# Optimization experiments

Hardware: AMD Instinct MI355X
Metric: run time of the kernel (lower is better)

The kernel has to match this reference:

```python
import jax, jax.numpy as jnp
import numpy as np

DIM = 192
NUM_HEADS = 4
B, H, W = 2, 256, 256
EPS = 1e-12  # torch F.normalize default eps


def setup_inputs() -> dict:
    key = jax.random.key(0)
    k1, k2, k3 = jax.random.split(key, 3)
    x = jax.random.normal(k1, (B, DIM, H, W), dtype=jnp.float32)
    # depthwise qkv conv: groups=DIM, each group maps 1 in-ch -> 3 out-ch; torch OIHW layout (3*DIM, 1, 3, 3)
    w_qkv = jax.random.normal(k2, (3 * DIM, 1, 3, 3), dtype=jnp.float32) * 0.1
    temperature = jnp.ones((NUM_HEADS, 1, 1), dtype=jnp.float32)
    # 1x1 projection conv, stored as [out, in]
    w_proj = jax.random.normal(k3, (DIM, DIM), dtype=jnp.float32) * (1.0 / np.sqrt(DIM))
    return {"x": x, "w_qkv": w_qkv, "temperature": temperature, "w_proj": w_proj}


def reference(x, w_qkv, temperature, w_proj):
    b, c, h, w = x.shape
    num_heads = temperature.shape[0]
    ch = c // num_heads  # channels per head
    # grouped (depthwise) 3x3 conv producing qkv; torch grouped-conv channel order
    # matches feature_group_count ordering (3 consecutive out-chs per group)... but
    # note torch chunk(3, dim=1) splits the 3*c output into contiguous thirds, so
    # q gets out-channels [0, c), etc. We replicate exactly with same layout.
    qkv = jax.lax.conv_general_dilated(
        x, w_qkv, window_strides=(1, 1), padding=((1, 1), (1, 1)),
        feature_group_count=c,
        dimension_numbers=("NCHW", "OIHW", "NCHW"))
    q, k, v = jnp.split(qkv, 3, axis=1)  # each [b, c, h, w]
    q = q.reshape(b, num_heads, ch, h * w)
    k = k.reshape(b, num_heads, ch, h * w)
    v = v.reshape(b, num_heads, ch, h * w)
    # L2 normalize along spatial dim (torch F.normalize with eps clamp)
    q = q / jnp.maximum(jnp.linalg.norm(q, axis=-1, keepdims=True), EPS)
    k = k / jnp.maximum(jnp.linalg.norm(k, axis=-1, keepdims=True), EPS)
    # channel-channel cosine attention, [b, head, ch, ch] (small)
    attn = jnp.einsum("bhcn,bhdn->bhcd", q, k) * temperature
    attn = jax.nn.softmax(attn, axis=-1)
    out = jnp.einsum("bhcd,bhdn->bhcn", attn, v).reshape(b, c, h, w)
    # 1x1 projection conv
    out = jnp.einsum("oi,bihw->bohw", w_proj, out)
    return out
```

## Files before the change

### kernel.cpp

```cpp
#include <hip/hip_runtime.h>
#include <math.h>

#define BB 2
#define CC 192
#define NH 4
#define CH 48
#define SRCP 16
#define HH 256
#define WW 256
#define NPIX (HH*WW)

typedef __attribute__((ext_vector_type(8))) short short8;
typedef __attribute__((ext_vector_type(4))) float f4;

static __device__ __forceinline__ unsigned short f2bf(float f) {
    union { float f; unsigned int u; } c; c.f = f;
    unsigned int r = c.u + 0x7fffu + ((c.u >> 16) & 1u);
    return (unsigned short)(r >> 16);
}

__global__ __launch_bounds__(256, 3) void k_conv(
    const float* __restrict__ x, const float* __restrict__ wqkv,
    unsigned short* __restrict__ vws, float* __restrict__ Sws,
    float* __restrict__ sqws)
{
    __shared__ unsigned int qk32[2][CH][132];

    const int tid = threadIdx.x;
    const int hd = blockIdx.x;
    const int y  = blockIdx.y;
    const int b  = blockIdx.z;

    {
        const int xp = tid;
        const int y0 = (y > 0) ? (y-1) : 0;
        const int y2 = (y < HH-1) ? (y+1) : y;
        const int xl = (xp > 0) ? (xp-1) : 0;
        const int xr = (xp < WW-1) ? (xp+1) : xp;
        const float my0 = (y > 0) ? 1.f : 0.f;
        const float my2 = (y < HH-1) ? 1.f : 0.f;
        const float mx0 = (xp > 0) ? 1.f : 0.f;
        const float mx2 = (xp < WW-1) ? 1.f : 0.f;
        const float m00 = my0*mx0, m02 = my0*mx2, m20 = my2*mx0, m22 = my2*mx2;

        #pragma unroll
        for (int type = 0; type < 2; ++type) {
            const int srcbase = type*64 + SRCP*hd;
            const float* wt = wqkv + type*(CC*9) + hd*(CH*9);
            for (int g4 = 0; g4 < SRCP; g4 += 4) {
                float A[4][9];
                #pragma unroll
                for (int u = 0; u < 4; ++u) {
                    const float* base = x + ((size_t)(b*CC + srcbase + g4 + u)*HH)*WW;
                    const float* r0 = base + (size_t)y0*WW;
                    const float* r1 = base + (size_t)y *WW;
                    const float* r2 = base + (size_t)y2*WW;
                    A[u][0] = r0[xl]; A[u][1] = r0[xp]; A[u][2] = r0[xr];
                    A[u][3] = r1[xl]; A[u][4] = r1[xp]; A[u][5] = r1[xr];
                    A[u][6] = r2[xl]; A[u][7] = r2[xp]; A[u][8] = r2[xr];
                }
                #pragma unroll
                for (int u = 0; u < 4; ++u) {
                    const int g = g4 + u;
                    float a00 = A[u][0]*m00, a01 = A[u][1]*my0, a02 = A[u][2]*m02;
                    float a10 = A[u][3]*mx0, a11 = A[u][4],     a12 = A[u][5]*mx2;
                    float a20 = A[u][6]*m20, a21 = A[u][7]*my2, a22 = A[u][8]*m22;
                    #pragma unroll
                    for (int r = 0; r < 3; ++r) {
                        const int cl = 3*g + r;
                        const float* w = wt + cl*9;
                        float val = a00*w[0] + a01*w[1] + a02*w[2]
                                  + a10*w[3] + a11*w[4] + a12*w[5]
                                  + a20*w[6] + a21*w[7] + a22*w[8];
                        ((unsigned short*)&qk32[type][cl][0])[xp] = f2bf(val);
                    }
                }
            }
        }

        unsigned int vpack[24];
        {
            const int srcbase = 128 + SRCP*hd;
            const float* wt = wqkv + 2*(CC*9) + hd*(CH*9);
            #pragma unroll
            for (int g4 = 0; g4 < SRCP; g4 += 4) {
                float A[4][9];
                #pragma unroll
                for (int u = 0; u < 4; ++u) {
                    const float* base = x + ((size_t)(b*CC + srcbase + g4 + u)*HH)*WW;
                    const float* r0 = base + (size_t)y0*WW;
                    const float* r1 = base + (size_t)y *WW;
                    const float* r2 = base + (size_t)y2*WW;
                    A[u][0] = r0[xl]; A[u][1] = r0[xp]; A[u][2] = r0[xr];
                    A[u][3] = r1[xl]; A[u][4] = r1[xp]; A[u][5] = r1[xr];
                    A[u][6] = r2[xl]; A[u][7] = r2[xp]; A[u][8] = r2[xr];
                }
                #pragma unroll
                for (int u = 0; u < 4; ++u) {
                    const int g = g4 + u;
                    float a00 = A[u][0]*m00, a01 = A[u][1]*my0, a02 = A[u][2]*m02;
                    float a10 = A[u][3]*mx0, a11 = A[u][4],     a12 = A[u][5]*mx2;
                    float a20 = A[u][6]*m20, a21 = A[u][7]*my2, a22 = A[u][8]*m22;
                    #pragma unroll
                    for (int r = 0; r < 3; ++r) {
                        const int cl = 3*g + r;
                        const float* w = wt + cl*9;
                        float val = a00*w[0] + a01*w[1] + a02*w[2]
                                  + a10*w[3] + a11*w[4] + a12*w[5]
                                  + a20*w[6] + a21*w[7] + a22*w[8];
                        unsigned int uu = f2bf(val);
                        if (cl & 1) vpack[cl >> 1] |= (uu << 16);
                        else        vpack[cl >> 1]  = uu;
                    }
                }
            }
        }
        {
            unsigned short* vp = vws + ((size_t)b*NPIX + (size_t)y*WW + xp)*CC + hd*CH;
            #pragma unroll
            for (int st = 0; st < 6; ++st) {
                uint4 u; u.x = vpack[st*4+0]; u.y = vpack[st*4+1];
                         u.z = vpack[st*4+2]; u.w = vpack[st*4+3];
                *(uint4*)(vp + st*8) = u;
            }
        }
    }
    __syncthreads();

    if (tid < 2*CH) {
        const int which = tid / CH;
        const int cl = tid - which*CH;
        const uint4* row = (const uint4*)&qk32[which][cl][0];
        float ssum = 0.f;
        for (int j = 0; j < 32; ++j) {
            uint4 u = row[j];
            #pragma unroll
            for (int q4 = 0; q4 < 4; ++q4) {
                unsigned int w = (&u.x)[q4];
                float lo = __uint_as_float(w << 16);
                float hi = __uint_as_float(w & 0xffff0000u);
                ssum = fmaf(lo, lo, ssum);
                ssum = fmaf(hi, hi, ssum);
            }
        }
        atomicAdd(&sqws[((b*NH + hd)*2 + which)*CH + cl], ssum);
    }

    {
        const int lane = tid & 63;
        const int wv = tid >> 6;
        const int m = lane & 15, quad = lane >> 4;
        for (int p = wv; p < 9; p += 4) {
            const int ct = p / 3, dt = p - ct*3;
            f4 acc = {0.f, 0.f, 0.f, 0.f};
            const char* qbase = (const char*)&qk32[0][ct*16 + m][0] + quad*16;
            const char* kbase = (const char*)&qk32[1][dt*16 + m][0] + quad*16;
            #pragma unroll
            for (int ks = 0; ks < 8; ++ks) {
                short8 afr = *(const short8*)(qbase + ks*64);
                short8 bfr = *(const short8*)(kbase + ks*64);
                acc = __builtin_amdgcn_mfma_f32_16x16x32_bf16(afr, bfr, acc, 0, 0, 0);
            }
            const int c0 = ct*16 + quad*4, d = dt*16 + m;
            float* Sp = Sws + ((size_t)(b*NH + hd)*CH + c0)*CH + d;
            #pragma unroll
            for (int r = 0; r < 4; ++r) atomicAdd(Sp + r*CH, acc[r]);
        }
    }
}

__global__ __launch_bounds__(256) void k_attn(
    const float* __restrict__ Sws, const float* __restrict__ sqws,
    const float* __restrict__ temp, const float* __restrict__ wproj,
    unsigned short* __restrict__ W2bf)
{
    __shared__ float att[CH][CH+1];
    __shared__ float wp[CC][CH+1];
    __shared__ float nrm[2][CH];

    const int tid = threadIdx.x;
    const int b  = blockIdx.x >> 2;
    const int hd = blockIdx.x & 3;

    if (tid < 2*CH) {
        int which = tid / CH, cl = tid - which*CH;
        nrm[which][cl] = fmaxf(sqrtf(sqws[((b*NH + hd)*2 + which)*CH + cl]), 1e-12f);
    }
    __syncthreads();

    const float tscale = temp[hd];
    for (int m = tid; m < CH*CH; m += 256) {
        int c = m / CH, d = m - c*CH;
        att[c][d] = Sws[((size_t)(b*NH + hd)*CH + c)*CH + d] * tscale
                    / (nrm[0][c] * nrm[1][d]);
    }
    __syncthreads();

    if (tid < CH) {
        float mx = -1e30f;
        for (int d = 0; d < CH; ++d) mx = fmaxf(mx, att[tid][d]);
        float sm = 0.f;
        for (int d = 0; d < CH; ++d) { float e = expf(att[tid][d] - mx); att[tid][d] = e; sm += e; }
        float inv = 1.f / sm;
        for (int d = 0; d < CH; ++d) att[tid][d] *= inv;
    }

    for (int m = tid; m < CC*CH; m += 256) {
        int o = m / CH, il = m - o*CH;
        wp[o][il] = wproj[o*CC + hd*CH + il];
    }
    __syncthreads();

    const int o0  = (tid & 31) * 6;
    const int dl0 = (tid >> 5) * 6;
    float a[6][6];
    #pragma unroll
    for (int i = 0; i < 6; ++i)
        #pragma unroll
        for (int j = 0; j < 6; ++j) a[i][j] = 0.f;
    for (int il = 0; il < CH; ++il) {
        float wv[6], av[6];
        #pragma unroll
        for (int i = 0; i < 6; ++i) wv[i] = wp[o0+i][il];
        #pragma unroll
        for (int j = 0; j < 6; ++j) av[j] = att[il][dl0+j];
        #pragma unroll
        for (int i = 0; i < 6; ++i)
            #pragma unroll
            for (int j = 0; j < 6; ++j)
                a[i][j] = fmaf(wv[i], av[j], a[i][j]);
    }
    #pragma unroll
    for (int i = 0; i < 6; ++i)
        #pragma unroll
        for (int j = 0; j < 6; ++j)
            W2bf[((size_t)b*CC + o0 + i)*CC + hd*CH + dl0 + j] = f2bf(a[i][j]);
}

__global__ __launch_bounds__(256, 4) void k_out(
    const unsigned short* __restrict__ vws, const unsigned short* __restrict__ W2bf,
    float* __restrict__ out)
{
    __shared__ unsigned short w2l[96][200];

    const int tid = threadIdx.x;
    const int b   = blockIdx.y;
    const int nblk = blockIdx.x >> 1;
    const int mh   = blockIdx.x & 1;
    const int n0 = nblk * 128;
    const int m_base = mh * 96;

    {
        for (int i = tid; i < 96*24; i += 256) {
            int o = i / 24, c = i - o*24;
            *(uint4*)&w2l[o][c*8] =
                ((const uint4*)(W2bf + ((size_t)(b*CC + m_base + o))*CC))[c];
        }
    }
    __syncthreads();

    const int lane = tid & 63;
    const int wv = tid >> 6;
    const int nn0 = wv * 32;
    const int m = lane & 15, quad = lane >> 4;

    f4 acc[6][2];
    #pragma unroll
    for (int mt = 0; mt < 6; ++mt)
        #pragma unroll
        for (int nt = 0; nt < 2; ++nt) acc[mt][nt] = (f4){0.f, 0.f, 0.f, 0.f};

    const unsigned short* vb = vws + ((size_t)b*NPIX + n0 + nn0 + m)*CC + quad*8;

    #pragma unroll
    for (int ks = 0; ks < 6; ++ks) {
        short8 bfr[2];
        #pragma unroll
        for (int nt = 0; nt < 2; ++nt)
            bfr[nt] = *(const short8*)(vb + (size_t)(nt*16)*CC + ks*32);
        #pragma unroll
        for (int mt = 0; mt < 6; ++mt) {
            short8 afr = *(const short8*)&w2l[mt*16 + m][ks*32 + quad*8];
            #pragma unroll
            for (int nt = 0; nt < 2; ++nt)
                acc[mt][nt] = __builtin_amdgcn_mfma_f32_16x16x32_bf16(afr, bfr[nt], acc[mt][nt], 0, 0, 0);
        }
    }

    float* trsp = (float*)w2l;
    const int orow = lane >> 2;
    const int seg  = (lane & 3) * 8;

    #pragma unroll
    for (int ph = 0; ph < 2; ++ph) {
        const int mtb = ph * 4;
        const int nmt = (ph == 0) ? 4 : 2;
        __syncthreads();
        #pragma unroll
        for (int mtl = 0; mtl < 4; ++mtl) {
            if (mtl >= nmt) break;
            #pragma unroll
            for (int nt = 0; nt < 2; ++nt)
                #pragma unroll
                for (int r = 0; r < 4; ++r)
                    trsp[((wv*4 + mtl)*16 + quad*4 + r)*34 + nt*16 + m] = acc[mtb+mtl][nt][r];
        }
        __syncthreads();
        #pragma unroll
        for (int mtl = 0; mtl < 4; ++mtl) {
            if (mtl >= nmt) break;
            const float* srcp = &trsp[((wv*4 + mtl)*16 + orow)*34 + seg];
            f4 d0 = *(const f4*)(srcp + 0);
            f4 d1 = *(const f4*)(srcp + 4);
            const int o = m_base + (mtb + mtl)*16 + orow;
            float* op = out + ((size_t)(b*CC + o))*NPIX + n0 + nn0 + seg;
            *(f4*)(op + 0) = d0;
            *(f4*)(op + 4) = d1;
        }
    }
}

extern "C" void kernel_launch(void* const* d_in, const int* in_sizes, int n_in,
                              void* d_out, int out_size, void* d_ws, size_t ws_size,
                              hipStream_t stream)
{
    const float* x     = (const float*)d_in[0];
    const float* wqkv  = (const float*)d_in[1];
    const float* temp  = (const float*)d_in[2];
    const float* wproj = (const float*)d_in[3];
    float* out = (float*)d_out;
    (void)in_sizes; (void)n_in; (void)out_size; (void)ws_size;

    unsigned short* vws = (unsigned short*)d_ws;
    const size_t VBYTES = (size_t)BB*CC*NPIX*sizeof(unsigned short);
    float* Sws  = (float*)((char*)d_ws + VBYTES);
    float* sqws = Sws + (size_t)BB*NH*CH*CH;
    unsigned short* W2bf = (unsigned short*)(sqws + (size_t)BB*NH*2*CH);

    hipMemsetAsync(Sws, 0, (size_t)(BB*NH*CH*CH + BB*NH*2*CH)*sizeof(float), stream);
    k_conv<<<dim3(NH, HH, BB), 256, 0, stream>>>(x, wqkv, vws, Sws, sqws);
    k_attn<<<dim3(BB*NH), 256, 0, stream>>>(Sws, sqws, temp, wproj, W2bf);
    k_out<<<dim3((NPIX/128)*2, BB), 256, 0, stream>>>(vws, W2bf, out);
}
```

Before: 298.9 us.

## Split conv work across two half-row blocks with per-thread channel halves

Each k_conv block now covers 128 pixels of a row rather than 256. The two halves of the thread block each compute half of the source-channel groups, so per-thread work and register use roughly halve. Shared memory per block drops, the grid doubles, and launch bounds raise the minimum blocks per SM to 6 to increase occupancy and latency hiding. In exchange, the atomic adds into the Gram matrix and the squared-norm buffer double in count, and per-block MFMA work shrinks.

```diff
diff --git a/kernel.cpp b/kernel.cpp
--- a/kernel.cpp
+++ b/kernel.cpp
@@ -19,20 +19,25 @@
     return (unsigned short)(r >> 16);
 }
 
-__global__ __launch_bounds__(256, 3) void k_conv(
+__global__ __launch_bounds__(256, 6) void k_conv(
     const float* __restrict__ x, const float* __restrict__ wqkv,
     unsigned short* __restrict__ vws, float* __restrict__ Sws,
     float* __restrict__ sqws)
 {
-    __shared__ unsigned int qk32[2][CH][132];
+    __shared__ unsigned int qk32[2][CH][68];
 
     const int tid = threadIdx.x;
     const int hd = blockIdx.x;
-    const int y  = blockIdx.y;
+    const int by = blockIdx.y;
     const int b  = blockIdx.z;
+    const int y  = by >> 1;
+    const int xh = by & 1;
+
+    const int pxl  = tid & 127;
+    const int half = tid >> 7;
+    const int xp   = xh*128 + pxl;
 
     {
-        const int xp = tid;
         const int y0 = (y > 0) ? (y-1) : 0;
         const int y2 = (y < HH-1) ? (y+1) : y;
         const int xl = (xp > 0) ? (xp-1) : 0;
@@ -47,7 +52,9 @@
         for (int type = 0; type < 2; ++type) {
             const int srcbase = type*64 + SRCP*hd;
             const float* wt = wqkv + type*(CC*9) + hd*(CH*9);
-            for (int g4 = 0; g4 < SRCP; g4 += 4) {
+            #pragma unroll
+            for (int gb = 0; gb < 2; ++gb) {
+                const int g4 = half*8 + gb*4;
                 float A[4][9];
                 #pragma unroll
                 for (int u = 0; u < 4; ++u) {
@@ -72,18 +79,19 @@
                         float val = a00*w[0] + a01*w[1] + a02*w[2]
                                   + a10*w[3] + a11*w[4] + a12*w[5]
                                   + a20*w[6] + a21*w[7] + a22*w[8];
-                        ((unsigned short*)&qk32[type][cl][0])[xp] = f2bf(val);
+                        ((unsigned short*)&qk32[type][cl][0])[pxl] = f2bf(val);
                     }
                 }
             }
         }
 
-        unsigned int vpack[24];
+        unsigned int vpack[12];
         {
             const int srcbase = 128 + SRCP*hd;
             const float* wt = wqkv + 2*(CC*9) + hd*(CH*9);
             #pragma unroll
-            for (int g4 = 0; g4 < SRCP; g4 += 4) {
+            for (int gb = 0; gb < 2; ++gb) {
+                const int g4 = half*8 + gb*4;
                 float A[4][9];
                 #pragma unroll
                 for (int u = 0; u < 4; ++u) {
@@ -103,22 +111,23 @@
                     float a20 = A[u][6]*m20, a21 = A[u][7]*my2, a22 = A[u][8]*m22;
                     #pragma unroll
                     for (int r = 0; r < 3; ++r) {
-                        const int cl = 3*g + r;
-                        const float* w = wt + cl*9;
+                        const int cll = 3*(gb*4 + u) + r;
+                        const float* w = wt + (3*g + r)*9;
                         float val = a00*w[0] + a01*w[1] + a02*w[2]
                                   + a10*w[3] + a11*w[4] + a12*w[5]
                                   + a20*w[6] + a21*w[7] + a22*w[8];
                         unsigned int uu = f2bf(val);
-                        if (cl & 1) vpack[cl >> 1] |= (uu << 16);
-                        else        vpack[cl >> 1]  = uu;
+                        if (cll & 1) vpack[cll >> 1] |= (uu << 16);
+                        else         vpack[cll >> 1]  = uu;
                     }
                 }
             }
         }
         {
-            unsigned short* vp = vws + ((size_t)b*NPIX + (size_t)y*WW + xp)*CC + hd*CH;
-            #pragma unroll
-            for (int st = 0; st < 6; ++st) {
+            unsigned short* vp = vws + ((size_t)b*NPIX + (size_t)y*WW + xp)*CC
+                                 + hd*CH + half*24;
+            #pragma unroll
+            for (int st = 0; st < 3; ++st) {
                 uint4 u; u.x = vpack[st*4+0]; u.y = vpack[st*4+1];
                          u.z = vpack[st*4+2]; u.w = vpack[st*4+3];
                 *(uint4*)(vp + st*8) = u;
@@ -132,7 +141,7 @@
         const int cl = tid - which*CH;
         const uint4* row = (const uint4*)&qk32[which][cl][0];
         float ssum = 0.f;
-        for (int j = 0; j < 32; ++j) {
+        for (int j = 0; j < 16; ++j) {
             uint4 u = row[j];
             #pragma unroll
             for (int q4 = 0; q4 < 4; ++q4) {
@@ -156,7 +165,7 @@
             const char* qbase = (const char*)&qk32[0][ct*16 + m][0] + quad*16;
             const char* kbase = (const char*)&qk32[1][dt*16 + m][0] + quad*16;
             #pragma unroll
-            for (int ks = 0; ks < 8; ++ks) {
+            for (int ks = 0; ks < 4; ++ks) {
                 short8 afr = *(const short8*)(qbase + ks*64);
                 short8 bfr = *(const short8*)(kbase + ks*64);
                 acc = __builtin_amdgcn_mfma_f32_16x16x32_bf16(afr, bfr, acc, 0, 0, 0);
@@ -338,7 +347,7 @@
     unsigned short* W2bf = (unsigned short*)(sqws + (size_t)BB*NH*2*CH);
 
     hipMemsetAsync(Sws, 0, (size_t)(BB*NH*CH*CH + BB*NH*2*CH)*sizeof(float), stream);
-    k_conv<<<dim3(NH, HH, BB), 256, 0, stream>>>(x, wqkv, vws, Sws, sqws);
+    k_conv<<<dim3(NH, HH*2, BB), 256, 0, stream>>>(x, wqkv, vws, Sws, sqws);
     k_attn<<<dim3(BB*NH), 256, 0, stream>>>(Sws, sqws, temp, wproj, W2bf);
     k_out<<<dim3((NPIX/128)*2, BB), 256, 0, stream>>>(vws, W2bf, out);
 }
```

Result: slower. 789.1 us (+164.0%).

## Split V-channel depthwise conv into its own kernel separate from QK conv

Applied to the files above, without the earlier changes.

Moves the V third of the depthwise qkv conv out of the QK conv+Gram kernel into a separate k_convv kernel. In k_convv each 256-thread block covers 64 pixels, and each of its four waves handles one head's 48 V channels. This makes the QK kernel lighter in registers and work per block, and lets V be computed with a different block shape. The cost is an extra kernel launch and a second read of the x rows in a separate pass.

```diff
diff --git a/kernel.cpp b/kernel.cpp
--- a/kernel.cpp
+++ b/kernel.cpp
@@ -19,10 +19,9 @@
     return (unsigned short)(r >> 16);
 }
 
-__global__ __launch_bounds__(256, 3) void k_conv(
+__global__ __launch_bounds__(256, 3) void k_convqk(
     const float* __restrict__ x, const float* __restrict__ wqkv,
-    unsigned short* __restrict__ vws, float* __restrict__ Sws,
-    float* __restrict__ sqws)
+    float* __restrict__ Sws, float* __restrict__ sqws)
 {
     __shared__ unsigned int qk32[2][CH][132];
 
@@ -77,53 +76,6 @@
                 }
             }
         }
-
-        unsigned int vpack[24];
-        {
-            const int srcbase = 128 + SRCP*hd;
-            const float* wt = wqkv + 2*(CC*9) + hd*(CH*9);
-            #pragma unroll
-            for (int g4 = 0; g4 < SRCP; g4 += 4) {
-                float A[4][9];
-                #pragma unroll
-                for (int u = 0; u < 4; ++u) {
-                    const float* base = x + ((size_t)(b*CC + srcbase + g4 + u)*HH)*WW;
-                    const float* r0 = base + (size_t)y0*WW;
-                    const float* r1 = base + (size_t)y *WW;
-                    const float* r2 = base + (size_t)y2*WW;
-                    A[u][0] = r0[xl]; A[u][1] = r0[xp]; A[u][2] = r0[xr];
-                    A[u][3] = r1[xl]; A[u][4] = r1[xp]; A[u][5] = r1[xr];
-                    A[u][6] = r2[xl]; A[u][7] = r2[xp]; A[u][8] = r2[xr];
-                }
-                #pragma unroll
-                for (int u = 0; u < 4; ++u) {
-                    const int g = g4 + u;
-                    float a00 = A[u][0]*m00, a01 = A[u][1]*my0, a02 = A[u][2]*m02;
-                    float a10 = A[u][3]*mx0, a11 = A[u][4],     a12 = A[u][5]*mx2;
-                    float a20 = A[u][6]*m20, a21 = A[u][7]*my2, a22 = A[u][8]*m22;
-                    #pragma unroll
-                    for (int r = 0; r < 3; ++r) {
-                        const int cl = 3*g + r;
-                        const float* w = wt + cl*9;
-                        float val = a00*w[0] + a01*w[1] + a02*w[2]
-                                  + a10*w[3] + a11*w[4] + a12*w[5]
-                                  + a20*w[6] + a21*w[7] + a22*w[8];
-                        unsigned int uu = f2bf(val);
-                        if (cl & 1) vpack[cl >> 1] |= (uu << 16);
-                        else        vpack[cl >> 1]  = uu;
-                    }
-                }
-            }
-        }
-        {
-            unsigned short* vp = vws + ((size_t)b*NPIX + (size_t)y*WW + xp)*CC + hd*CH;
-            #pragma unroll
-            for (int st = 0; st < 6; ++st) {
-                uint4 u; u.x = vpack[st*4+0]; u.y = vpack[st*4+1];
-                         u.z = vpack[st*4+2]; u.w = vpack[st*4+3];
-                *(uint4*)(vp + st*8) = u;
-            }
-        }
     }
     __syncthreads();
 
@@ -169,6 +121,74 @@
     }
 }
 
+__global__ __launch_bounds__(256) void k_convv(
+    const float* __restrict__ x, const float* __restrict__ wqkv,
+    unsigned short* __restrict__ vws)
+{
+    const int tid  = threadIdx.x;
+    const int lane = tid & 63;
+    const int s    = tid >> 6;
+    const int xp = blockIdx.x*64 + lane;
+    const int y  = blockIdx.y;
+    const int b  = blockIdx.z;
+
+    const int y0 = (y > 0) ? (y-1) : 0;
+    const int y2 = (y < HH-1) ? (y+1) : y;
+    const int xl = (xp > 0) ? (xp-1) : 0;
+    const int xr = (xp < WW-1) ? (xp+1) : xp;
+    const float my0 = (y > 0) ? 1.f : 0.f;
+    const float my2 = (y < HH-1) ? 1.f : 0.f;
+    const float mx0 = (xp > 0) ? 1.f : 0.f;
+    const float mx2 = (xp < WW-1) ? 1.f : 0.f;
+    const float m00 = my0*mx0, m02 = my0*mx2, m20 = my2*mx0, m22 = my2*mx2;
+
+    unsigned int vpack[24];
+    const float* wt = wqkv + 2*(CC*9);
+
+    #pragma unroll
+    for (int gb = 0; gb < 4; ++gb) {
+        const int g4 = s*16 + gb*4;
+        float A[4][9];
+        #pragma unroll
+        for (int u = 0; u < 4; ++u) {
+            const float* base = x + ((size_t)(b*CC + 128 + g4 + u)*HH)*WW;
+            const float* r0 = base + (size_t)y0*WW;
+            const float* r1 = base + (size_t)y *WW;
+            const float* r2 = base + (size_t)y2*WW;
+            A[u][0] = r0[xl]; A[u][1] = r0[xp]; A[u][2] = r0[xr];
+            A[u][3] = r1[xl]; A[u][4] = r1[xp]; A[u][5] = r1[xr];
+            A[u][6] = r2[xl]; A[u][7] = r2[xp]; A[u][8] = r2[xr];
+        }
+        #pragma unroll
+        for (int u = 0; u < 4; ++u) {
+            const int gc = g4 + u;
+            float a00 = A[u][0]*m00, a01 = A[u][1]*my0, a02 = A[u][2]*m02;
+            float a10 = A[u][3]*mx0, a11 = A[u][4],     a12 = A[u][5]*mx2;
+            float a20 = A[u][6]*m20, a21 = A[u][7]*my2, a22 = A[u][8]*m22;
+            #pragma unroll
+            for (int r = 0; r < 3; ++r) {
+                const int cll = 3*(gb*4 + u) + r;
+                const float* w = wt + (3*gc + r)*9;
+                float val = a00*w[0] + a01*w[1] + a02*w[2]
+                          + a10*w[3] + a11*w[4] + a12*w[5]
+                          + a20*w[6] + a21*w[7] + a22*w[8];
+                unsigned int uu = f2bf(val);
+                if (cll & 1) vpack[cll >> 1] |= (uu << 16);
+                else         vpack[cll >> 1]  = uu;
+            }
+        }
+    }
+    {
+        unsigned short* vp = vws + ((size_t)b*NPIX + (size_t)y*WW + xp)*CC + s*48;
+        #pragma unroll
+        for (int st = 0; st < 6; ++st) {
+            uint4 u; u.x = vpack[st*4+0]; u.y = vpack[st*4+1];
+                     u.z = vpack[st*4+2]; u.w = vpack[st*4+3];
+            *(uint4*)(vp + st*8) = u;
+        }
+    }
+}
+
 __global__ __launch_bounds__(256) void k_attn(
     const float* __restrict__ Sws, const float* __restrict__ sqws,
     const float* __restrict__ temp, const float* __restrict__ wproj,
@@ -338,7 +358,8 @@
     unsigned short* W2bf = (unsigned short*)(sqws + (size_t)BB*NH*2*CH);
 
     hipMemsetAsync(Sws, 0, (size_t)(BB*NH*CH*CH + BB*NH*2*CH)*sizeof(float), stream);
-    k_conv<<<dim3(NH, HH, BB), 256, 0, stream>>>(x, wqkv, vws, Sws, sqws);
+    k_convqk<<<dim3(NH, HH, BB), 256, 0, stream>>>(x, wqkv, Sws, sqws);
+    k_convv<<<dim3(WW/64, HH, BB), 256, 0, stream>>>(x, wqkv, vws);
     k_attn<<<dim3(BB*NH), 256, 0, stream>>>(Sws, sqws, temp, wproj, W2bf);
     k_out<<<dim3((NPIX/128)*2, BB), 256, 0, stream>>>(vws, W2bf, out);
 }
```

Result: slower. 319.6 us (+6.9%).
